# Optimization experiments

Hardware: AMD Instinct MI355X
Metric: run time of the kernel (lower is better)

The kernel has to match this reference:

```python
import jax, jax.numpy as jnp
import numpy as np

D_MODEL = 768
KAN_HIDDEN = 2048
NUM_CP = 16        # number of B-spline control points / coefficients per edge
DEGREE = 3         # cubic splines
RMIN, RMAX = -4.0, 4.0


def bspline_basis(x, num_cp=NUM_CP, degree=DEGREE, rmin=RMIN, rmax=RMAX):
    """Cox-de Boor B-spline basis.
    x: (N, D) -> basis: (N, D, num_cp). Uniform knots extended by `degree`
    on each side so that [rmin, rmax] has full basis support.
    """
    h = (rmax - rmin) / (num_cp - degree)
    # K = num_cp + degree + 1 knots
    knots = rmin - degree * h + jnp.arange(num_cp + degree + 1, dtype=x.dtype) * h
    xe = x[..., None]  # (N, D, 1)
    # degree-0 indicator bases: (N, D, num_cp + degree)
    b = ((xe >= knots[:-1]) & (xe < knots[1:])).astype(x.dtype)
    for d in range(1, degree + 1):
        t0 = knots[:-(d + 1)]   # t[k]
        t1 = knots[d:-1]        # t[k+d]
        t2 = knots[d + 1:]      # t[k+d+1]
        t3 = knots[1:-d]        # t[k+1]
        b = (xe - t0) / (t1 - t0) * b[..., :-1] + (t2 - xe) / (t2 - t3) * b[..., 1:]
    return b  # (N, D, num_cp)


def kan_layer(x, w):
    """x: (N, Din); w: (Dout, Din, num_cp) per-edge spline coefficients."""
    basis = bspline_basis(x)                      # (N, Din, K)
    return jnp.einsum('ndk,odk->no', basis, w)    # (N, Dout)


def setup_inputs() -> dict:
    key = jax.random.key(0)
    kx, k1, k2 = jax.random.split(key, 3)
    x = jax.random.normal(kx, (2, 2048, D_MODEL), dtype=jnp.float32)
    # spline coefficient tables, small init like nn.init scaled normal
    w1 = jax.random.normal(k1, (KAN_HIDDEN, D_MODEL, NUM_CP), dtype=jnp.float32) * (1.0 / np.sqrt(D_MODEL * NUM_CP))
    w2 = jax.random.normal(k2, (D_MODEL, KAN_HIDDEN, NUM_CP), dtype=jnp.float32) * (1.0 / np.sqrt(KAN_HIDDEN * NUM_CP))
    return {"x": x, "w1": w1, "w2": w2}


def reference(x, w1, w2):
    B, T, D = x.shape
    input_dtype = x.dtype
    h = x.reshape(B * T, D).astype(jnp.float32)
    h = kan_layer(h, w1)                # (B*T, KAN_HIDDEN)
    h = kan_layer(h, w2)                # (B*T, D_MODEL)
    h = h.astype(input_dtype)
    # dropout p=0.0 / eval mode -> identity
    return h.reshape(B, T, -1)
```

## Files before the change

### kernel.cpp

```cpp
#include <hip/hip_runtime.h>
#include <stdint.h>

typedef __attribute__((ext_vector_type(8))) short short8;
typedef __attribute__((ext_vector_type(4))) float f32x4;
typedef __attribute__((ext_vector_type(4))) int i32x4;

#define DMODEL 768
#define HID    2048
#define MROWS  4096

#define KINVH  (13.0f/8.0f)
#define KNOT0  (-4.0f - 3.0f*(8.0f/13.0f))

__device__ __forceinline__ unsigned short f2bf(float f) {
  unsigned int u = __float_as_uint(f);
  unsigned int r = (u + 0x7FFFu + ((u >> 16) & 1u)) >> 16;
  return (unsigned short)r;
}

template<int DIN>
__global__ void __launch_bounds__(256) conv_pack(const float* __restrict__ src,
                                                 unsigned short* __restrict__ dst,
                                                 int total_waves) {
  constexpr int NK2 = DIN / 2;
  int gw = blockIdx.x * 4 + (threadIdx.x >> 6);
  if (gw >= total_waves) return;
  int l   = threadIdx.x & 63;
  int cb  = gw / NK2;
  int kt2 = gw % NK2;
  int c16 = l & 15, q = l >> 4;
  int col = cb * 16 + c16;
  const float* s = src + ((size_t)col * DIN + kt2 * 2 + (q >> 1)) * 16 + (q & 1) * 8;
  float4 v0 = *(const float4*)s;
  float4 v1 = *(const float4*)(s + 4);
  short8 o;
  o[0] = (short)f2bf(v0.x); o[1] = (short)f2bf(v0.y);
  o[2] = (short)f2bf(v0.z); o[3] = (short)f2bf(v0.w);
  o[4] = (short)f2bf(v1.x); o[5] = (short)f2bf(v1.y);
  o[6] = (short)f2bf(v1.z); o[7] = (short)f2bf(v1.w);
  unsigned short* d = dst + (((size_t)cb * NK2 + kt2) * 64 + q * 16 + c16) * 8;
  *(short8*)d = o;
}

__global__ void __launch_bounds__(256) reduce2(float4* __restrict__ p, int n4) {
  int i = blockIdx.x * 256 + threadIdx.x;
  if (i >= n4) return;
  float4 a = p[i], b = p[i + n4];
  float4 r;
  r.x = a.x + b.x; r.y = a.y + b.y; r.z = a.z + b.z; r.w = a.w + b.w;
  p[i] = r;
}

__global__ void __launch_bounds__(256) reduce4(const float4* __restrict__ p,
                                               float4* __restrict__ out, int n4) {
  int i = blockIdx.x * 256 + threadIdx.x;
  if (i >= n4) return;
  float4 a = p[i], b = p[i + n4], c = p[i + 2 * n4], d = p[i + 3 * n4];
  float4 r;
  r.x = a.x + b.x + c.x + d.x;
  r.y = a.y + b.y + c.y + d.y;
  r.z = a.z + b.z + c.z + d.z;
  r.w = a.w + b.w + c.w + d.w;
  out[i] = r;
}

template<int DIN, int DOUT, int SPLITK>
__global__ void __launch_bounds__(256, 4)
kan_gemm(const float* __restrict__ X, const unsigned short* __restrict__ Wb,
         float* __restrict__ Out) {
  constexpr int BM  = 64;
  constexpr int BN  = 256;
  constexpr int NK  = (DIN * 16) / 64;
  constexpr int NK2 = DIN / 2;
  constexpr int NKS = NK / SPLITK;
  constexpr int GX  = MROWS / BM;
  constexpr int GY  = DOUT / BN;
  constexpr int CPX = (GX * GY) / 8;
  __shared__ __align__(16) char smA[BM * 128];

  const int tid  = threadIdx.x;
  const int lane = tid & 63;
  const int wid  = tid >> 6;

  const int d    = blockIdx.x + blockIdx.y * GX;
  const int lf   = (d & 7) * CPX + (d >> 3);
  const int brow = (lf % GX) * BM;
  const int bcol = (lf / GX) * BN;
  const int kt0  = blockIdx.z * NKS;
  const int kt1  = kt0 + NKS;

  f32x4 acc[4][4];
#pragma unroll
  for (int m = 0; m < 4; ++m)
#pragma unroll
    for (int n = 0; n < 4; ++n) acc[m][n] = (f32x4){0.f, 0.f, 0.f, 0.f};

  int a_base[4], a_sw[4];
#pragma unroll
  for (int m = 0; m < 4; ++m) {
    int row   = m * 16 + (lane & 15);
    a_base[m] = row * 128 + ((lane >> 4) * 16);
    a_sw[m]   = (row & 7) << 4;
  }

  const unsigned short* bp[4];
#pragma unroll
  for (int n = 0; n < 4; ++n)
    bp[n] = Wb + ((size_t)(bcol / 16 + wid * 4 + n) * NK2 + (size_t)kt0 * 2) * 512
               + lane * 8;

  const int br_ = tid >> 2;
  const int bd_ = tid & 3;
  const float* xrow = X + (size_t)(brow + br_) * DIN + bd_;

  float xcur = xrow[(size_t)kt0 * 4];
  short8 bv[2][4];
#pragma unroll
  for (int n = 0; n < 4; ++n) {
    bv[0][n] = *(const short8*)(bp[n]);
    bv[1][n] = *(const short8*)(bp[n] + 512);
    bp[n] += 1024;
  }

  for (int kt = kt0; kt < kt1; ++kt) {
    __syncthreads();

    {
      float u  = (xcur - KNOT0) * KINVH;
      float uf = floorf(u);
      int   jj = (int)uf;
      float t  = u - uf;
      float t2 = t * t, t3 = t2 * t;
      float p0 = (1.0f / 6.0f) * (1.0f - 3.0f * t + 3.0f * t2 - t3);
      float p1 = (1.0f / 6.0f) * (4.0f - 6.0f * t2 + 3.0f * t3);
      float p2 = (1.0f / 6.0f) * (1.0f + 3.0f * t + 3.0f * t2 - 3.0f * t3);
      float p3 = (1.0f / 6.0f) * t3;

      int base = br_ * 128 + bd_ * 32;
      int sw   = (br_ & 7) << 4;
      *(i32x4*)(smA + (base ^ sw))        = (i32x4){0, 0, 0, 0};
      *(i32x4*)(smA + ((base + 16) ^ sw)) = (i32x4){0, 0, 0, 0};
      unsigned short q0 = f2bf(p0), q1 = f2bf(p1), q2 = f2bf(p2), q3 = f2bf(p3);
      int k0 = jj - 3;
      if ((unsigned)(k0 + 0) < 16u) *(unsigned short*)(smA + ((base + (k0 + 0) * 2) ^ sw)) = q0;
      if ((unsigned)(k0 + 1) < 16u) *(unsigned short*)(smA + ((base + (k0 + 1) * 2) ^ sw)) = q1;
      if ((unsigned)(k0 + 2) < 16u) *(unsigned short*)(smA + ((base + (k0 + 2) * 2) ^ sw)) = q2;
      if ((unsigned)(k0 + 3) < 16u) *(unsigned short*)(smA + ((base + (k0 + 3) * 2) ^ sw)) = q3;
    }

    {
      int ktn = (kt + 1 < kt1) ? kt + 1 : kt;
      xcur = xrow[(size_t)ktn * 4];
    }

    __syncthreads();

#pragma unroll
    for (int kk = 0; kk < 2; ++kk) {
      short8 a[4];
#pragma unroll
      for (int m = 0; m < 4; ++m)
        a[m] = *(const short8*)(smA + ((a_base[m] + kk * 64) ^ a_sw[m]));
#pragma unroll
      for (int m = 0; m < 4; ++m)
#pragma unroll
        for (int n = 0; n < 4; ++n)
          acc[m][n] = __builtin_amdgcn_mfma_f32_16x16x32_bf16(a[m], bv[kk][n], acc[m][n], 0, 0, 0);
    }

    if (kt + 1 < kt1) {
#pragma unroll
      for (int n = 0; n < 4; ++n) {
        bv[0][n] = *(const short8*)(bp[n]);
        bv[1][n] = *(const short8*)(bp[n] + 512);
        bp[n] += 1024;
      }
    }
  }

  float* outp = Out + (size_t)blockIdx.z * MROWS * DOUT;
#pragma unroll
  for (int m = 0; m < 4; ++m)
#pragma unroll
    for (int n = 0; n < 4; ++n)
#pragma unroll
      for (int q = 0; q < 4; ++q) {
        int grow = brow + m * 16 + (lane >> 4) * 4 + q;
        int gcol = bcol + wid * 64 + n * 16 + (lane & 15);
        outp[(size_t)grow * DOUT + gcol] = acc[m][n][q];
      }
}

extern "C" void kernel_launch(void* const* d_in, const int* in_sizes, int n_in,
                              void* d_out, int out_size, void* d_ws, size_t ws_size,
                              hipStream_t stream) {
  const float* x  = (const float*)d_in[0];
  const float* w1 = (const float*)d_in[1];
  const float* w2 = (const float*)d_in[2];
  float* out = (float*)d_out;

  char* ws = (char*)d_ws;
  unsigned short* wgb   = (unsigned short*)ws;
  float*          part1 = (float*)(ws + 50331648);
  float*          hbf   = part1;
  float*          part2 = (float*)(ws + 83886080);

  {
    const int waves = (HID / 16) * (DMODEL / 2);
    conv_pack<DMODEL><<<waves / 4, 256, 0, stream>>>(w1, wgb, waves);
  }
  kan_gemm<DMODEL, HID, 2>
      <<<dim3(MROWS / 64, HID / 256, 2), 256, 0, stream>>>(x, wgb, part1);
  const int hn4 = (MROWS * HID) / 4;
  reduce2<<<hn4 / 256, 256, 0, stream>>>((float4*)part1, hn4);

  {
    const int waves = (DMODEL / 16) * (HID / 2);
    conv_pack<HID><<<waves / 4, 256, 0, stream>>>(w2, wgb, waves);
  }
  kan_gemm<HID, DMODEL, 4>
      <<<dim3(MROWS / 64, DMODEL / 256, 4), 256, 0, stream>>>(hbf, wgb, part2);
  const int rn4 = (MROWS * DMODEL) / 4;
  reduce4<<<rn4 / 256, 256, 0, stream>>>((const float4*)part2, (float4*)out, rn4);
}
```

Before: 454.5 us.

## Double the GEMM K-tile and fuse the w2 pack with the split-K reduce

Each main-loop iteration now covers 8 input features (K=128) instead of 4. The LDS A-tile grows to 16 KB with a 16-row XOR swizzle, and the second half of the B fragments is loaded partway through the iteration. This halves the number of barrier pairs and basis-generation phases per tile, at the cost of more LDS per block and more live registers. The w2 bf16 pack and the first split-K reduction now run as one launch, removing a kernel launch. The bf16 conversion uses the HIP intrinsic, and the cubic basis weights are computed in a factored (1-t) form.

```diff
diff --git a/kernel.cpp b/kernel.cpp
--- a/kernel.cpp
+++ b/kernel.cpp
@@ -1,4 +1,5 @@
 #include <hip/hip_runtime.h>
+#include <hip/hip_bf16.h>
 #include <stdint.h>
 
 typedef __attribute__((ext_vector_type(8))) short short8;
@@ -13,18 +14,14 @@
 #define KNOT0  (-4.0f - 3.0f*(8.0f/13.0f))
 
 __device__ __forceinline__ unsigned short f2bf(float f) {
-  unsigned int u = __float_as_uint(f);
-  unsigned int r = (u + 0x7FFFu + ((u >> 16) & 1u)) >> 16;
-  return (unsigned short)r;
+  __hip_bfloat16 h = __float2bfloat16(f);
+  return *reinterpret_cast<unsigned short*>(&h);
 }
 
 template<int DIN>
-__global__ void __launch_bounds__(256) conv_pack(const float* __restrict__ src,
-                                                 unsigned short* __restrict__ dst,
-                                                 int total_waves) {
+__device__ __forceinline__ void pack_wave(const float* __restrict__ src,
+                                          unsigned short* __restrict__ dst, int gw) {
   constexpr int NK2 = DIN / 2;
-  int gw = blockIdx.x * 4 + (threadIdx.x >> 6);
-  if (gw >= total_waves) return;
   int l   = threadIdx.x & 63;
   int cb  = gw / NK2;
   int kt2 = gw % NK2;
@@ -38,17 +35,30 @@
   o[2] = (short)f2bf(v0.z); o[3] = (short)f2bf(v0.w);
   o[4] = (short)f2bf(v1.x); o[5] = (short)f2bf(v1.y);
   o[6] = (short)f2bf(v1.z); o[7] = (short)f2bf(v1.w);
-  unsigned short* d = dst + (((size_t)cb * NK2 + kt2) * 64 + q * 16 + c16) * 8;
-  *(short8*)d = o;
-}
-
-__global__ void __launch_bounds__(256) reduce2(float4* __restrict__ p, int n4) {
-  int i = blockIdx.x * 256 + threadIdx.x;
-  if (i >= n4) return;
-  float4 a = p[i], b = p[i + n4];
-  float4 r;
-  r.x = a.x + b.x; r.y = a.y + b.y; r.z = a.z + b.z; r.w = a.w + b.w;
-  p[i] = r;
+  *(short8*)(dst + (((size_t)cb * NK2 + kt2) * 64 + q * 16 + c16) * 8) = o;
+}
+
+__global__ void __launch_bounds__(256) conv_pack1(const float* __restrict__ src,
+                                                  unsigned short* __restrict__ dst) {
+  pack_wave<DMODEL>(src, dst, blockIdx.x * 4 + (threadIdx.x >> 6));
+}
+
+__global__ void __launch_bounds__(256) pack2_reduce2(const float* __restrict__ w2,
+                                                     unsigned short* __restrict__ dst,
+                                                     float4* __restrict__ p, int n4) {
+  constexpr int PACK_BLOCKS = ((DMODEL / 16) * (HID / 2)) / 4;
+  int b = blockIdx.x;
+  if (b < PACK_BLOCKS) {
+    pack_wave<HID>(w2, dst, b * 4 + (threadIdx.x >> 6));
+  } else {
+    int i = (b - PACK_BLOCKS) * 256 + threadIdx.x;
+    if (i < n4) {
+      float4 a = p[i], q = p[i + n4];
+      float4 r;
+      r.x = a.x + q.x; r.y = a.y + q.y; r.z = a.z + q.z; r.w = a.w + q.w;
+      p[i] = r;
+    }
+  }
 }
 
 __global__ void __launch_bounds__(256) reduce4(const float4* __restrict__ p,
@@ -70,13 +80,13 @@
          float* __restrict__ Out) {
   constexpr int BM  = 64;
   constexpr int BN  = 256;
-  constexpr int NK  = (DIN * 16) / 64;
+  constexpr int NK  = (DIN * 16) / 128;
   constexpr int NK2 = DIN / 2;
   constexpr int NKS = NK / SPLITK;
   constexpr int GX  = MROWS / BM;
   constexpr int GY  = DOUT / BN;
   constexpr int CPX = (GX * GY) / 8;
-  __shared__ __align__(16) char smA[BM * 128];
+  __shared__ __align__(16) char smA[BM * 256];
 
   const int tid  = threadIdx.x;
   const int lane = tid & 63;
@@ -95,85 +105,112 @@
 #pragma unroll
     for (int n = 0; n < 4; ++n) acc[m][n] = (f32x4){0.f, 0.f, 0.f, 0.f};
 
-  int a_base[4], a_sw[4];
-#pragma unroll
-  for (int m = 0; m < 4; ++m) {
-    int row   = m * 16 + (lane & 15);
-    a_base[m] = row * 128 + ((lane >> 4) * 16);
-    a_sw[m]   = (row & 7) << 4;
-  }
+  const int aswz0 = (((lane & 15) * 256) + ((lane >> 4) * 16)) ^ ((lane & 15) << 4);
 
   const unsigned short* bp[4];
 #pragma unroll
   for (int n = 0; n < 4; ++n)
-    bp[n] = Wb + ((size_t)(bcol / 16 + wid * 4 + n) * NK2 + (size_t)kt0 * 2) * 512
+    bp[n] = Wb + ((size_t)(bcol / 16 + wid * 4 + n) * NK2 + (size_t)kt0 * 4) * 512
                + lane * 8;
 
-  const int br_ = tid >> 2;
-  const int bd_ = tid & 3;
+  const int br_ = tid >> 3;
+  const int bd_ = tid & 7;
   const float* xrow = X + (size_t)(brow + br_) * DIN + bd_;
-
-  float xcur = xrow[(size_t)kt0 * 4];
+  constexpr size_t XO2 = (size_t)32 * DIN;
+
+  auto BASIS = [&](float xv, int row) {
+    float u  = (xv - KNOT0) * KINVH;
+    float uf = floorf(u);
+    int   jj = (int)uf;
+    float t  = u - uf;
+    float s1 = 1.0f - t;
+    float t2 = t * t, t3 = t2 * t;
+    float s2 = s1 * s1, s3 = s2 * s1;
+    float p0 = s3 * (1.0f / 6.0f);
+    float p3 = t3 * (1.0f / 6.0f);
+    float p1 = fmaf(0.5f, t3, 2.0f / 3.0f) - t2;
+    float p2 = fmaf(0.5f, s3, 2.0f / 3.0f) - s2;
+
+    int base = row * 256 + bd_ * 32;
+    int sw   = (row & 15) << 4;
+    *(i32x4*)(smA + (base ^ sw))        = (i32x4){0, 0, 0, 0};
+    *(i32x4*)(smA + ((base + 16) ^ sw)) = (i32x4){0, 0, 0, 0};
+    unsigned short q0 = f2bf(p0), q1 = f2bf(p1), q2 = f2bf(p2), q3 = f2bf(p3);
+    int k0 = jj - 3;
+    if ((unsigned)(k0 + 0) < 16u) *(unsigned short*)(smA + ((base + (k0 + 0) * 2) ^ sw)) = q0;
+    if ((unsigned)(k0 + 1) < 16u) *(unsigned short*)(smA + ((base + (k0 + 1) * 2) ^ sw)) = q1;
+    if ((unsigned)(k0 + 2) < 16u) *(unsigned short*)(smA + ((base + (k0 + 2) * 2) ^ sw)) = q2;
+    if ((unsigned)(k0 + 3) < 16u) *(unsigned short*)(smA + ((base + (k0 + 3) * 2) ^ sw)) = q3;
+  };
+
+  float xc0 = xrow[(size_t)kt0 * 8];
+  float xc1 = xrow[(size_t)kt0 * 8 + XO2];
   short8 bv[2][4];
 #pragma unroll
   for (int n = 0; n < 4; ++n) {
     bv[0][n] = *(const short8*)(bp[n]);
     bv[1][n] = *(const short8*)(bp[n] + 512);
-    bp[n] += 1024;
   }
 
   for (int kt = kt0; kt < kt1; ++kt) {
     __syncthreads();
 
-    {
-      float u  = (xcur - KNOT0) * KINVH;
-      float uf = floorf(u);
-      int   jj = (int)uf;
-      float t  = u - uf;
-      float t2 = t * t, t3 = t2 * t;
-      float p0 = (1.0f / 6.0f) * (1.0f - 3.0f * t + 3.0f * t2 - t3);
-      float p1 = (1.0f / 6.0f) * (4.0f - 6.0f * t2 + 3.0f * t3);
-      float p2 = (1.0f / 6.0f) * (1.0f + 3.0f * t + 3.0f * t2 - 3.0f * t3);
-      float p3 = (1.0f / 6.0f) * t3;
-
-      int base = br_ * 128 + bd_ * 32;
-      int sw   = (br_ & 7) << 4;
-      *(i32x4*)(smA + (base ^ sw))        = (i32x4){0, 0, 0, 0};
-      *(i32x4*)(smA + ((base + 16) ^ sw)) = (i32x4){0, 0, 0, 0};
-      unsigned short q0 = f2bf(p0), q1 = f2bf(p1), q2 = f2bf(p2), q3 = f2bf(p3);
-      int k0 = jj - 3;
-      if ((unsigned)(k0 + 0) < 16u) *(unsigned short*)(smA + ((base + (k0 + 0) * 2) ^ sw)) = q0;
-      if ((unsigned)(k0 + 1) < 16u) *(unsigned short*)(smA + ((base + (k0 + 1) * 2) ^ sw)) = q1;
-      if ((unsigned)(k0 + 2) < 16u) *(unsigned short*)(smA + ((base + (k0 + 2) * 2) ^ sw)) = q2;
-      if ((unsigned)(k0 + 3) < 16u) *(unsigned short*)(smA + ((base + (k0 + 3) * 2) ^ sw)) = q3;
-    }
-
+    BASIS(xc0, br_);
+    BASIS(xc1, br_ + 32);
     {
       int ktn = (kt + 1 < kt1) ? kt + 1 : kt;
-      xcur = xrow[(size_t)ktn * 4];
+      xc0 = xrow[(size_t)ktn * 8];
+      xc1 = xrow[(size_t)ktn * 8 + XO2];
     }
 
     __syncthreads();
 
-#pragma unroll
-    for (int kk = 0; kk < 2; ++kk) {
-      short8 a[4];
-#pragma unroll
-      for (int m = 0; m < 4; ++m)
-        a[m] = *(const short8*)(smA + ((a_base[m] + kk * 64) ^ a_sw[m]));
-#pragma unroll
-      for (int m = 0; m < 4; ++m)
-#pragma unroll
-        for (int n = 0; n < 4; ++n)
-          acc[m][n] = __builtin_amdgcn_mfma_f32_16x16x32_bf16(a[m], bv[kk][n], acc[m][n], 0, 0, 0);
-    }
+    short8 a[4];
+#pragma unroll
+    for (int m = 0; m < 4; ++m)
+      a[m] = *(const short8*)(smA + (aswz0 ^ 0) + m * 4096);
+#pragma unroll
+    for (int m = 0; m < 4; ++m)
+#pragma unroll
+      for (int n = 0; n < 4; ++n)
+        acc[m][n] = __builtin_amdgcn_mfma_f32_16x16x32_bf16(a[m], bv[0][n], acc[m][n], 0, 0, 0);
+#pragma unroll
+    for (int m = 0; m < 4; ++m)
+      a[m] = *(const short8*)(smA + (aswz0 ^ 64) + m * 4096);
+#pragma unroll
+    for (int m = 0; m < 4; ++m)
+#pragma unroll
+      for (int n = 0; n < 4; ++n)
+        acc[m][n] = __builtin_amdgcn_mfma_f32_16x16x32_bf16(a[m], bv[1][n], acc[m][n], 0, 0, 0);
+
+#pragma unroll
+    for (int n = 0; n < 4; ++n) {
+      bv[0][n] = *(const short8*)(bp[n] + 1024);
+      bv[1][n] = *(const short8*)(bp[n] + 1536);
+    }
+#pragma unroll
+    for (int m = 0; m < 4; ++m)
+      a[m] = *(const short8*)(smA + (aswz0 ^ 128) + m * 4096);
+#pragma unroll
+    for (int m = 0; m < 4; ++m)
+#pragma unroll
+      for (int n = 0; n < 4; ++n)
+        acc[m][n] = __builtin_amdgcn_mfma_f32_16x16x32_bf16(a[m], bv[0][n], acc[m][n], 0, 0, 0);
+#pragma unroll
+    for (int m = 0; m < 4; ++m)
+      a[m] = *(const short8*)(smA + (aswz0 ^ 192) + m * 4096);
+#pragma unroll
+    for (int m = 0; m < 4; ++m)
+#pragma unroll
+      for (int n = 0; n < 4; ++n)
+        acc[m][n] = __builtin_amdgcn_mfma_f32_16x16x32_bf16(a[m], bv[1][n], acc[m][n], 0, 0, 0);
 
     if (kt + 1 < kt1) {
 #pragma unroll
       for (int n = 0; n < 4; ++n) {
+        bp[n] += 2048;
         bv[0][n] = *(const short8*)(bp[n]);
         bv[1][n] = *(const short8*)(bp[n] + 512);
-        bp[n] += 1024;
       }
     }
   }
@@ -205,18 +242,15 @@
   float*          hbf   = part1;
   float*          part2 = (float*)(ws + 83886080);
 
-  {
-    const int waves = (HID / 16) * (DMODEL / 2);
-    conv_pack<DMODEL><<<waves / 4, 256, 0, stream>>>(w1, wgb, waves);
-  }
+  conv_pack1<<<((HID / 16) * (DMODEL / 2)) / 4, 256, 0, stream>>>(w1, wgb);
   kan_gemm<DMODEL, HID, 2>
       <<<dim3(MROWS / 64, HID / 256, 2), 256, 0, stream>>>(x, wgb, part1);
-  const int hn4 = (MROWS * HID) / 4;
-  reduce2<<<hn4 / 256, 256, 0, stream>>>((float4*)part1, hn4);
 
   {
-    const int waves = (DMODEL / 16) * (HID / 2);
-    conv_pack<HID><<<waves / 4, 256, 0, stream>>>(w2, wgb, waves);
+    const int hn4 = (MROWS * HID) / 4;
+    const int packB = ((DMODEL / 16) * (HID / 2)) / 4;
+    const int redB  = hn4 / 256;
+    pack2_reduce2<<<packB + redB, 256, 0, stream>>>(w2, wgb, (float4*)part1, hn4);
   }
   kan_gemm<HID, DMODEL, 4>
       <<<dim3(MROWS / 64, DMODEL / 256, 4), 256, 0, stream>>>(hbf, wgb, part2);
```

Measured after the change: 478.5 us. 1.05x slower.
